# Optimization experiments

Measured on AMD Instinct MI355X. Metric: run time of the kernel, lower is better.

The kernel has to match this reference:

```python
import jax, jax.numpy as jnp
import numpy as np

D_MODEL = 1024
NUM_HEADS = 16
B, S = 1, 4096


def setup_inputs() -> dict:
    key = jax.random.key(0)
    kx, kq, kk, kv, ko = jax.random.split(key, 5)
    std = (1.0 / D_MODEL) ** 0.5
    def trunc(k):
        return std * jax.random.truncated_normal(k, -3.0, 3.0, (D_MODEL, D_MODEL), dtype=jnp.float32)
    return {
        "x": jax.random.normal(kx, (B, S, D_MODEL), dtype=jnp.float32),
        "W_Q": trunc(kq),
        "W_K": trunc(kk),
        "W_V": trunc(kv),
        "W_O": trunc(ko),
    }


def reference(x, W_Q, W_K, W_V, W_O):
    Bx, Sx, Dm = x.shape
    H = NUM_HEADS
    d_attn = Dm // H
    # projections (torch code uses x @ W.T)
    Q = x @ W_Q.T
    K = x @ W_K.T
    V = x @ W_V.T
    # [B, H, S, d]
    Q = Q.reshape(Bx, Sx, H, d_attn).transpose(0, 2, 1, 3)
    K = K.reshape(Bx, Sx, H, d_attn).transpose(0, 2, 1, 3)
    V = V.reshape(Bx, Sx, H, d_attn).transpose(0, 2, 1, 3)
    scale = 1.0 / jnp.sqrt(jnp.asarray(d_attn, dtype=x.dtype))
    # [B, H, S, S] scores
    attn = jnp.einsum("bhqd,bhkd->bhqk", Q, K) * scale
    causal = jnp.tril(jnp.ones((Sx, Sx), dtype=bool))
    attn = jnp.where(causal, attn, jnp.asarray(-jnp.inf, dtype=attn.dtype))
    probs = jax.nn.softmax(attn, axis=-1)
    y = jnp.einsum("bhqk,bhkd->bhqd", probs, V)
    y = y.transpose(0, 2, 1, 3).reshape(Bx, Sx, Dm)
    return y @ W_O.T
```

## Files before the change

### kernel.cpp

```cpp
#include <hip/hip_runtime.h>

#define S_LEN 4096
#define DMODEL 1024
#define NHEADS 16

typedef __attribute__((ext_vector_type(8))) short bf16x8;
typedef __attribute__((ext_vector_type(4))) float f32x4;
typedef unsigned short u16;
typedef unsigned int u32;
typedef unsigned long long u64;

__device__ inline u16 f2bf(float f) {
    union { float f; u32 u; } v; v.f = f;
    u32 r = v.u + 0x7fffu + ((v.u >> 16) & 1u);
    return (u16)(r >> 16);
}

__device__ inline u32 pkbf2(float a, float b) {
    union { float f; u32 u; } ua, ub; ua.f = a; ub.f = b;
    const u32 ra = ua.u + 0x7fffu + ((ua.u >> 16) & 1u);
    const u32 rb = ub.u + 0x7fffu + ((ub.u >> 16) & 1u);
    return __builtin_amdgcn_perm(rb, ra, 0x07060302u);
}

__device__ inline u32 pkbf2f(float a, float b) {
    union { float f; u32 u; } ua, ub; ua.f = a; ub.f = b;
    const u32 ra = ua.u + 0x8000u;
    const u32 rb = ub.u + 0x8000u;
    return __builtin_amdgcn_perm(rb, ra, 0x07060302u);
}

__device__ inline void cp16(const void* g, void* l) {
    __builtin_amdgcn_global_load_lds(
        (const __attribute__((address_space(1))) unsigned int*)g,
        (__attribute__((address_space(3))) unsigned int*)l, 16, 0, 0);
}

__global__ __launch_bounds__(256) void cvt_all(const float* __restrict__ x,
                                               const float* __restrict__ wq,
                                               const float* __restrict__ wk,
                                               const float* __restrict__ wv,
                                               const float* __restrict__ wo,
                                               u16* __restrict__ xb,
                                               u16* __restrict__ w3,
                                               u16* __restrict__ wob) {
    const int b = blockIdx.x;
    const float* s; u16* d; int off;
    const int NW = DMODEL * DMODEL;
    if (b < 2048)      { s = x;  d = xb;          off = b * 2048; }
    else if (b < 2560) { s = wq; d = w3;          off = (b - 2048) * 2048; }
    else if (b < 3072) { s = wk; d = w3 + NW;     off = (b - 2560) * 2048; }
    else if (b < 3584) { s = wv; d = w3 + 2 * NW; off = (b - 3072) * 2048; }
    else               { s = wo; d = wob;         off = (b - 3584) * 2048; }
    const int i = off + threadIdx.x * 8;
    const float4 a = *(const float4*)(s + i);
    const float4 c = *(const float4*)(s + i + 4);
    u16 t[8];
    t[0] = f2bf(a.x); t[1] = f2bf(a.y); t[2] = f2bf(a.z); t[3] = f2bf(a.w);
    t[4] = f2bf(c.x); t[5] = f2bf(c.y); t[6] = f2bf(c.z); t[7] = f2bf(c.w);
    *(bf16x8*)(d + i) = *(const bf16x8*)t;
}

__global__ __launch_bounds__(256) void gemm_qkv(const u16* __restrict__ A,
                                                const u16* __restrict__ B3,
                                                u16* __restrict__ Qo,
                                                u16* __restrict__ Ko,
                                                u16* __restrict__ Vo) {
    __shared__ __align__(16) u16 As[2][128 * 32];
    __shared__ __align__(16) u16 Bs[2][128 * 32];
    const int tid = threadIdx.x, lane = tid & 63, wave = tid >> 6;
    const int wm = (wave >> 1) * 64, wn = (wave & 1) * 64;
    const int m0 = blockIdx.y * 128, n0 = blockIdx.x * 128;
    const int l15 = lane & 15, quad = lane >> 4;

    f32x4 acc[4][4];
#pragma unroll
    for (int i = 0; i < 4; i++)
#pragma unroll
        for (int j = 0; j < 4; j++) acc[i][j] = (f32x4){0.f, 0.f, 0.f, 0.f};

    const int r0 = tid >> 2, c0 = (tid & 3) * 8;

    cp16(A + (size_t)(m0 + r0) * 1024 + c0,       As[0] + r0 * 32 + c0);
    cp16(A + (size_t)(m0 + r0 + 64) * 1024 + c0,  As[0] + (r0 + 64) * 32 + c0);
    cp16(B3 + (size_t)(n0 + r0) * 1024 + c0,      Bs[0] + r0 * 32 + c0);
    cp16(B3 + (size_t)(n0 + r0 + 64) * 1024 + c0, Bs[0] + (r0 + 64) * 32 + c0);

    int cur = 0;
    for (int kk = 0; kk < 1024; kk += 32) {
        __syncthreads();
        if (kk + 32 < 1024) {
            const int kn = kk + 32;
            cp16(A + (size_t)(m0 + r0) * 1024 + kn + c0,       As[cur ^ 1] + r0 * 32 + c0);
            cp16(A + (size_t)(m0 + r0 + 64) * 1024 + kn + c0,  As[cur ^ 1] + (r0 + 64) * 32 + c0);
            cp16(B3 + (size_t)(n0 + r0) * 1024 + kn + c0,      Bs[cur ^ 1] + r0 * 32 + c0);
            cp16(B3 + (size_t)(n0 + r0 + 64) * 1024 + kn + c0, Bs[cur ^ 1] + (r0 + 64) * 32 + c0);
        }
        bf16x8 af[4], bfr[4];
#pragma unroll
        for (int i = 0; i < 4; i++)
            af[i] = *(const bf16x8*)(As[cur] + (wm + i * 16 + l15) * 32 + quad * 8);
#pragma unroll
        for (int j = 0; j < 4; j++)
            bfr[j] = *(const bf16x8*)(Bs[cur] + (wn + j * 16 + l15) * 32 + quad * 8);
#pragma unroll
        for (int i = 0; i < 4; i++)
#pragma unroll
            for (int j = 0; j < 4; j++)
                acc[i][j] = __builtin_amdgcn_mfma_f32_16x16x32_bf16(af[i], bfr[j], acc[i][j], 0, 0, 0);
        cur ^= 1;
    }

    const int which = n0 >> 10;
    const int n0r = n0 & 1023;
    u16* dst = (which == 0) ? Qo : (which == 1) ? Ko : Vo;
    const float sc = (which == 0) ? 0.125f * 1.4426950408889634f : 1.0f;
#pragma unroll
    for (int i = 0; i < 4; i++)
#pragma unroll
        for (int j = 0; j < 4; j++)
#pragma unroll
            for (int r = 0; r < 4; r++) {
                const int row = m0 + wm + i * 16 + quad * 4 + r;
                const int col = n0r + wn + j * 16 + l15;
                const int h = col >> 6, c = col & 63;
                const u16 v = f2bf(acc[i][j][r] * sc);
                if (which < 2) dst[(size_t)h * S_LEN * 64 + (size_t)row * 64 + c] = v;
                else           dst[(size_t)h * S_LEN * 64 + (size_t)c * S_LEN + row] = v;
            }
}

__global__ __launch_bounds__(256) void gemm_out(const u16* __restrict__ A,
                                                const u16* __restrict__ B,
                                                float* __restrict__ C) {
    __shared__ __align__(16) u16 As[2][64 * 64];
    __shared__ __align__(16) u16 Bs[2][128 * 64];
    const int tid = threadIdx.x, lane = tid & 63, wave = tid >> 6;
    const int wm = (wave >> 1) * 32, wn = (wave & 1) * 64;
    const int bx = blockIdx.x;
    const int n0 = (bx & 7) * 128, m0 = (bx >> 3) * 64;
    const int l15 = lane & 15, quad = lane >> 4;
    const int swz = l15 & 7;

    f32x4 acc[2][4];
#pragma unroll
    for (int i = 0; i < 2; i++)
#pragma unroll
        for (int j = 0; j < 4; j++) acc[i][j] = (f32x4){0.f, 0.f, 0.f, 0.f};

#define STAGE_OUT(buf, kb)                                                              \
    {                                                                                   \
        _Pragma("unroll")                                                               \
        for (int q = 0; q < 2; q++) {                                                   \
            const int ch = tid + q * 256;                                               \
            const int ar = ch >> 3, ac = ((ch & 7) ^ (ar & 7)) * 8;                     \
            cp16(A + (size_t)(m0 + ar) * 1024 + (kb) + ac, As[buf] + ch * 8);           \
        }                                                                               \
        _Pragma("unroll")                                                               \
        for (int q = 0; q < 4; q++) {                                                   \
            const int ch = tid + q * 256;                                               \
            const int br = ch >> 3, bc = ((ch & 7) ^ (br & 7)) * 8;                     \
            cp16(B + (size_t)(n0 + br) * 1024 + (kb) + bc, Bs[buf] + ch * 8);           \
        }                                                                               \
    }

    STAGE_OUT(0, 0);
    int cur = 0;
    for (int kk = 0; kk < 1024; kk += 64) {
        __syncthreads();
        if (kk + 64 < 1024) STAGE_OUT(cur ^ 1, kk + 64);
#pragma unroll
        for (int h = 0; h < 2; h++) {
            const int cc = (h * 4 + quad) ^ swz;
            bf16x8 af[2], bfr[4];
#pragma unroll
            for (int i = 0; i < 2; i++)
                af[i] = *(const bf16x8*)(As[cur] + (wm + i * 16 + l15) * 64 + cc * 8);
#pragma unroll
            for (int j = 0; j < 4; j++)
                bfr[j] = *(const bf16x8*)(Bs[cur] + (wn + j * 16 + l15) * 64 + cc * 8);
#pragma unroll
            for (int i = 0; i < 2; i++)
#pragma unroll
                for (int j = 0; j < 4; j++)
                    acc[i][j] = __builtin_amdgcn_mfma_f32_16x16x32_bf16(af[i], bfr[j], acc[i][j], 0, 0, 0);
        }
        cur ^= 1;
    }
#undef STAGE_OUT

#pragma unroll
    for (int i = 0; i < 2; i++)
#pragma unroll
        for (int j = 0; j < 4; j++)
#pragma unroll
            for (int r = 0; r < 4; r++) {
                const int row = m0 + wm + i * 16 + quad * 4 + r;
                const int col = n0 + wn + j * 16 + l15;
                C[(size_t)row * 1024 + col] = acc[i][j][r];
            }
}

__global__ __launch_bounds__(256, 2) void attn(const u16* __restrict__ Q,
                                               const u16* __restrict__ Kh,
                                               const u16* __restrict__ Vt,
                                               u16* __restrict__ Y) {
    __shared__ __align__(16) u16 Ks[2][128 * 64];
    __shared__ __align__(16) u16 Vs[2][64 * 128];
    const int b = blockIdx.x;
    const int head = b & 15;
    const int jq = 63 - (b >> 4);
    const int nkt = jq + 1;
    const int np = (nkt + 1) >> 1;
    const int qa = jq * 64;
    const int tid = threadIdx.x, lane = tid & 63, w = tid >> 6;
    const int l15 = lane & 15, quad = lane >> 4;
    const int swz = l15 & 7;

    const u16* Qp = Q + (size_t)head * S_LEN * 64;
    const u16* Kp = Kh + (size_t)head * S_LEN * 64;
    const u16* Vp = Vt + (size_t)head * 64 * S_LEN;

    bf16x8 qf[4][2];
#pragma unroll
    for (int qg = 0; qg < 4; qg++)
#pragma unroll
        for (int h = 0; h < 2; h++)
            qf[qg][h] = *(const bf16x8*)(Qp + (size_t)(qa + qg * 16 + l15) * 64 + h * 32 + quad * 8);

    f32x4 o[4][4];
#pragma unroll
    for (int dg = 0; dg < 4; dg++)
#pragma unroll
        for (int qg = 0; qg < 4; qg++) o[dg][qg] = (f32x4){0.f, 0.f, 0.f, 0.f};
    float lp[4] = {0.f, 0.f, 0.f, 0.f};

#define STAGE_PAIR(buf, kp2)                                                       \
    {                                                                              \
        _Pragma("unroll")                                                          \
        for (int q = 0; q < 4; q++) {                                              \
            const int ch = tid + q * 256;                                          \
            const int kr = ch >> 3, kc = ((ch & 7) ^ (kr & 7)) * 8;                \
            cp16(Kp + (size_t)((kp2) * 128 + kr) * 64 + kc, Ks[buf] + ch * 8);     \
            const int vr = ch >> 4, lc = ch & 15;                                  \
            const int vc = ((lc & 8) | ((lc & 7) ^ (vr & 7))) * 8;                 \
            cp16(Vp + (size_t)vr * S_LEN + (kp2) * 128 + vc, Vs[buf] + ch * 8);    \
        }                                                                          \
    }

    STAGE_PAIR(0, 0);
    int cur = 0;
    for (int kp = 0; kp < np; kp++) {
        __syncthreads();
        if (kp + 1 < np) STAGE_PAIR(cur ^ 1, kp + 1);
        const u16* K_ = Ks[cur];
        const u16* V_ = Vs[cur];
        const bool hasO = (2 * kp + 1 < nkt);
        const bool diagE = (2 * kp == jq);
        const bool diagO = (2 * kp + 1 == jq);

        const int rE = w * 16 + l15;
        const bf16x8 kE0 = *(const bf16x8*)(K_ + rE * 64 + (quad ^ swz) * 8);
        const bf16x8 kE1 = *(const bf16x8*)(K_ + rE * 64 + ((4 + quad) ^ swz) * 8);
        bf16x8 kO0, kO1;
        if (hasO) {
            kO0 = *(const bf16x8*)(K_ + (rE + 64) * 64 + (quad ^ swz) * 8);
            kO1 = *(const bf16x8*)(K_ + (rE + 64) * 64 + ((4 + quad) ^ swz) * 8);
        }

        const int keyl = w * 16 + quad * 4;
        union { u32 d[4]; bf16x8 v; } pu[4];
#pragma unroll
        for (int qg = 0; qg < 4; qg++) {
            const int ql = qg * 16 + l15;
            f32x4 cE = (f32x4){0.f, 0.f, 0.f, 0.f};
            cE = __builtin_amdgcn_mfma_f32_16x16x32_bf16(kE0, qf[qg][0], cE, 0, 0, 0);
            cE = __builtin_amdgcn_mfma_f32_16x16x32_bf16(kE1, qf[qg][1], cE, 0, 0, 0);
            float p0 = __builtin_amdgcn_exp2f(cE[0]);
            float p1 = __builtin_amdgcn_exp2f(cE[1]);
            float p2 = __builtin_amdgcn_exp2f(cE[2]);
            float p3 = __builtin_amdgcn_exp2f(cE[3]);
            if (diagE) {
                if (keyl + 0 > ql) p0 = 0.f;
                if (keyl + 1 > ql) p1 = 0.f;
                if (keyl + 2 > ql) p2 = 0.f;
                if (keyl + 3 > ql) p3 = 0.f;
            }
            lp[qg] += (p0 + p1) + (p2 + p3);
            pu[qg].d[0] = pkbf2f(p0, p1);
            pu[qg].d[1] = pkbf2f(p2, p3);
            if (hasO) {
                f32x4 cO = (f32x4){0.f, 0.f, 0.f, 0.f};
                cO = __builtin_amdgcn_mfma_f32_16x16x32_bf16(kO0, qf[qg][0], cO, 0, 0, 0);
                cO = __builtin_amdgcn_mfma_f32_16x16x32_bf16(kO1, qf[qg][1], cO, 0, 0, 0);
                float q0 = __builtin_amdgcn_exp2f(cO[0]);
                float q1 = __builtin_amdgcn_exp2f(cO[1]);
                float q2 = __builtin_amdgcn_exp2f(cO[2]);
                float q3 = __builtin_amdgcn_exp2f(cO[3]);
                if (diagO) {
                    if (keyl + 0 > ql) q0 = 0.f;
                    if (keyl + 1 > ql) q1 = 0.f;
                    if (keyl + 2 > ql) q2 = 0.f;
                    if (keyl + 3 > ql) q3 = 0.f;
                }
                lp[qg] += (q0 + q1) + (q2 + q3);
                pu[qg].d[2] = pkbf2f(q0, q1);
                pu[qg].d[3] = pkbf2f(q2, q3);
            } else {
                pu[qg].d[2] = 0u;
                pu[qg].d[3] = 0u;
            }
        }

#pragma unroll
        for (int dg = 0; dg < 4; dg++) {
            const int vrow = dg * 16 + l15;
            const int gcE = w * 2 + (quad >> 1);
            const int sc = gcE ^ swz;
            union { u64 d[2]; bf16x8 v; } vf;
            vf.d[0] = *(const u64*)(V_ + vrow * 128 + sc * 8 + (quad & 1) * 4);
            vf.d[1] = hasO ? *(const u64*)(V_ + vrow * 128 + (8 | sc) * 8 + (quad & 1) * 4)
                           : 0ull;
#pragma unroll
            for (int qg = 0; qg < 4; qg++)
                o[dg][qg] = __builtin_amdgcn_mfma_f32_16x16x32_bf16(vf.v, pu[qg].v, o[dg][qg], 0, 0, 0);
        }
        cur ^= 1;
    }
#undef STAGE_PAIR

#pragma unroll
    for (int qg = 0; qg < 4; qg++) {
        lp[qg] += __shfl_xor(lp[qg], 16);
        lp[qg] += __shfl_xor(lp[qg], 32);
    }
    __syncthreads();
    float* OR = (float*)&Ks[0][0];
    float* LR = (float*)&Vs[0][0];
    if (lane < 16) {
#pragma unroll
        for (int qg = 0; qg < 4; qg++) LR[(w * 4 + qg) * 16 + lane] = lp[qg];
    }
#pragma unroll
    for (int c = 0; c < 2; c++) {
        if (c) __syncthreads();
#pragma unroll
        for (int d2 = 0; d2 < 2; d2++)
#pragma unroll
            for (int qg = 0; qg < 4; qg++)
                *(f32x4*)&OR[(((w * 2 + d2) * 4 + qg) * 16 + l15) * 16 + quad * 4] = o[c * 2 + d2][qg];
        __syncthreads();
        const int d2r = w >> 1, qh = w & 1;
        const int qrow = qh * 32 + (lane >> 1);
        const int qg = qrow >> 4, lq = qrow & 15;
        const int dd = (lane & 1) * 8;
        f32x4 sa = (f32x4){0.f, 0.f, 0.f, 0.f};
        f32x4 sb = (f32x4){0.f, 0.f, 0.f, 0.f};
#pragma unroll
        for (int sw = 0; sw < 4; sw++) {
            const float* p = &OR[(((sw * 2 + d2r) * 4 + qg) * 16 + lq) * 16 + dd];
            sa += *(const f32x4*)p;
            sb += *(const f32x4*)(p + 4);
        }
        const float l = LR[qg * 16 + lq] + LR[(4 + qg) * 16 + lq] +
                        LR[(8 + qg) * 16 + lq] + LR[(12 + qg) * 16 + lq];
        const float inv = 1.f / l;
        const int dg = c * 2 + d2r;
        union { u32 d[4]; bf16x8 v; } yv;
        yv.d[0] = pkbf2(sa[0] * inv, sa[1] * inv);
        yv.d[1] = pkbf2(sa[2] * inv, sa[3] * inv);
        yv.d[2] = pkbf2(sb[0] * inv, sb[1] * inv);
        yv.d[3] = pkbf2(sb[2] * inv, sb[3] * inv);
        *(bf16x8*)(Y + (size_t)(qa + qrow) * DMODEL + head * 64 + dg * 16 + dd) = yv.v;
    }
}

extern "C" void kernel_launch(void* const* d_in, const int* in_sizes, int n_in,
                              void* d_out, int out_size, void* d_ws, size_t ws_size,
                              hipStream_t stream) {
    const float* x  = (const float*)d_in[0];
    const float* wq = (const float*)d_in[1];
    const float* wk = (const float*)d_in[2];
    const float* wv = (const float*)d_in[3];
    const float* wo = (const float*)d_in[4];
    float* out = (float*)d_out;

    u16* qh  = (u16*)d_ws;
    u16* kh  = qh + (size_t)S_LEN * DMODEL;
    u16* vt  = kh + (size_t)S_LEN * DMODEL;
    u16* xb  = vt + (size_t)S_LEN * DMODEL;
    u16* y   = xb;
    u16* wb3 = xb + (size_t)S_LEN * DMODEL;
    u16* wob = wb3 + (size_t)3 * DMODEL * DMODEL;

    const dim3 blk(256);

    cvt_all<<<4096, blk, 0, stream>>>(x, wq, wk, wv, wo, xb, wb3, wob);
    gemm_qkv<<<dim3(3 * DMODEL / 128, S_LEN / 128), blk, 0, stream>>>(xb, wb3, qh, kh, vt);
    attn<<<1024, blk, 0, stream>>>(qh, kh, vt, y);
    gemm_out<<<512, blk, 0, stream>>>(y, wob, out);
}
```

Baseline: 206.5 us.

## Load K and V fragments directly from global memory, drop LDS double-buffering

```diff
diff --git a/kernel.cpp b/kernel.cpp
--- a/kernel.cpp
+++ b/kernel.cpp
@@ -201,12 +201,12 @@
             }
 }
 
-__global__ __launch_bounds__(256, 2) void attn(const u16* __restrict__ Q,
+__global__ __launch_bounds__(256, 3) void attn(const u16* __restrict__ Q,
                                                const u16* __restrict__ Kh,
                                                const u16* __restrict__ Vt,
                                                u16* __restrict__ Y) {
-    __shared__ __align__(16) u16 Ks[2][128 * 64];
-    __shared__ __align__(16) u16 Vs[2][64 * 128];
+    __shared__ __align__(16) float OR[256 * 20];
+    __shared__ float LR[256];
     const int b = blockIdx.x;
     const int head = b & 15;
     const int jq = 63 - (b >> 4);
@@ -215,7 +215,6 @@
     const int qa = jq * 64;
     const int tid = threadIdx.x, lane = tid & 63, w = tid >> 6;
     const int l15 = lane & 15, quad = lane >> 4;
-    const int swz = l15 & 7;
 
     const u16* Qp = Q + (size_t)head * S_LEN * 64;
     const u16* Kp = Kh + (size_t)head * S_LEN * 64;
@@ -235,51 +234,37 @@
         for (int qg = 0; qg < 4; qg++) o[dg][qg] = (f32x4){0.f, 0.f, 0.f, 0.f};
     float lp[4] = {0.f, 0.f, 0.f, 0.f};
 
-#define STAGE_PAIR(buf, kp2)                                                       \
-    {                                                                              \
-        _Pragma("unroll")                                                          \
-        for (int q = 0; q < 4; q++) {                                              \
-            const int ch = tid + q * 256;                                          \
-            const int kr = ch >> 3, kc = ((ch & 7) ^ (kr & 7)) * 8;                \
-            cp16(Kp + (size_t)((kp2) * 128 + kr) * 64 + kc, Ks[buf] + ch * 8);     \
-            const int vr = ch >> 4, lc = ch & 15;                                  \
-            const int vc = ((lc & 8) | ((lc & 7) ^ (vr & 7))) * 8;                 \
-            cp16(Vp + (size_t)vr * S_LEN + (kp2) * 128 + vc, Vs[buf] + ch * 8);    \
-        }                                                                          \
-    }
-
-    STAGE_PAIR(0, 0);
-    int cur = 0;
+    const u16* kpe = Kp + (size_t)(w * 16 + l15) * 64 + quad * 8;
+    const u16* vp0 = Vp + (size_t)l15 * S_LEN + w * 16 + quad * 4;
+    const u16* vp1 = vp0 + (size_t)16 * S_LEN;
+    const u16* vp2 = vp0 + (size_t)32 * S_LEN;
+    const u16* vp3 = vp0 + (size_t)48 * S_LEN;
+
+    const int keyl = w * 16 + quad * 4;
+
     for (int kp = 0; kp < np; kp++) {
-        __syncthreads();
-        if (kp + 1 < np) STAGE_PAIR(cur ^ 1, kp + 1);
-        const u16* K_ = Ks[cur];
-        const u16* V_ = Vs[cur];
+        const bf16x8 kE0 = *(const bf16x8*)(kpe);
+        const bf16x8 kE1 = *(const bf16x8*)(kpe + 32);
+        const bf16x8 kO0 = *(const bf16x8*)(kpe + 64 * 64);
+        const bf16x8 kO1 = *(const bf16x8*)(kpe + 64 * 64 + 32);
+        kpe += 128 * 64;
         const bool hasO = (2 * kp + 1 < nkt);
         const bool diagE = (2 * kp == jq);
         const bool diagO = (2 * kp + 1 == jq);
 
-        const int rE = w * 16 + l15;
-        const bf16x8 kE0 = *(const bf16x8*)(K_ + rE * 64 + (quad ^ swz) * 8);
-        const bf16x8 kE1 = *(const bf16x8*)(K_ + rE * 64 + ((4 + quad) ^ swz) * 8);
-        bf16x8 kO0, kO1;
-        if (hasO) {
-            kO0 = *(const bf16x8*)(K_ + (rE + 64) * 64 + (quad ^ swz) * 8);
-            kO1 = *(const bf16x8*)(K_ + (rE + 64) * 64 + ((4 + quad) ^ swz) * 8);
-        }
-
-        const int keyl = w * 16 + quad * 4;
-        union { u32 d[4]; bf16x8 v; } pu[4];
+        union VU { u64 d[2]; bf16x8 v; };
+        union PU { u32 d[4]; bf16x8 v; } pu[4];
+
 #pragma unroll
         for (int qg = 0; qg < 4; qg++) {
             const int ql = qg * 16 + l15;
-            f32x4 cE = (f32x4){0.f, 0.f, 0.f, 0.f};
-            cE = __builtin_amdgcn_mfma_f32_16x16x32_bf16(kE0, qf[qg][0], cE, 0, 0, 0);
-            cE = __builtin_amdgcn_mfma_f32_16x16x32_bf16(kE1, qf[qg][1], cE, 0, 0, 0);
-            float p0 = __builtin_amdgcn_exp2f(cE[0]);
-            float p1 = __builtin_amdgcn_exp2f(cE[1]);
-            float p2 = __builtin_amdgcn_exp2f(cE[2]);
-            float p3 = __builtin_amdgcn_exp2f(cE[3]);
+            f32x4 c = (f32x4){0.f, 0.f, 0.f, 0.f};
+            c = __builtin_amdgcn_mfma_f32_16x16x32_bf16(kE0, qf[qg][0], c, 0, 0, 0);
+            c = __builtin_amdgcn_mfma_f32_16x16x32_bf16(kE1, qf[qg][1], c, 0, 0, 0);
+            float p0 = __builtin_amdgcn_exp2f(c[0]);
+            float p1 = __builtin_amdgcn_exp2f(c[1]);
+            float p2 = __builtin_amdgcn_exp2f(c[2]);
+            float p3 = __builtin_amdgcn_exp2f(c[3]);
             if (diagE) {
                 if (keyl + 0 > ql) p0 = 0.f;
                 if (keyl + 1 > ql) p1 = 0.f;
@@ -289,89 +274,86 @@
             lp[qg] += (p0 + p1) + (p2 + p3);
             pu[qg].d[0] = pkbf2f(p0, p1);
             pu[qg].d[1] = pkbf2f(p2, p3);
-            if (hasO) {
-                f32x4 cO = (f32x4){0.f, 0.f, 0.f, 0.f};
-                cO = __builtin_amdgcn_mfma_f32_16x16x32_bf16(kO0, qf[qg][0], cO, 0, 0, 0);
-                cO = __builtin_amdgcn_mfma_f32_16x16x32_bf16(kO1, qf[qg][1], cO, 0, 0, 0);
-                float q0 = __builtin_amdgcn_exp2f(cO[0]);
-                float q1 = __builtin_amdgcn_exp2f(cO[1]);
-                float q2 = __builtin_amdgcn_exp2f(cO[2]);
-                float q3 = __builtin_amdgcn_exp2f(cO[3]);
+        }
+
+        VU v0, v1, v2, v3;
+        v0.d[0] = *(const u64*)(vp0); v0.d[1] = *(const u64*)(vp0 + 64); vp0 += 128;
+        v1.d[0] = *(const u64*)(vp1); v1.d[1] = *(const u64*)(vp1 + 64); vp1 += 128;
+
+        if (hasO) {
+#pragma unroll
+            for (int qg = 0; qg < 4; qg++) {
+                const int ql = qg * 16 + l15;
+                f32x4 c = (f32x4){0.f, 0.f, 0.f, 0.f};
+                c = __builtin_amdgcn_mfma_f32_16x16x32_bf16(kO0, qf[qg][0], c, 0, 0, 0);
+                c = __builtin_amdgcn_mfma_f32_16x16x32_bf16(kO1, qf[qg][1], c, 0, 0, 0);
+                float p0 = __builtin_amdgcn_exp2f(c[0]);
+                float p1 = __builtin_amdgcn_exp2f(c[1]);
+                float p2 = __builtin_amdgcn_exp2f(c[2]);
+                float p3 = __builtin_amdgcn_exp2f(c[3]);
                 if (diagO) {
-                    if (keyl + 0 > ql) q0 = 0.f;
-                    if (keyl + 1 > ql) q1 = 0.f;
-                    if (keyl + 2 > ql) q2 = 0.f;
-                    if (keyl + 3 > ql) q3 = 0.f;
+                    if (keyl + 0 > ql) p0 = 0.f;
+                    if (keyl + 1 > ql) p1 = 0.f;
+                    if (keyl + 2 > ql) p2 = 0.f;
+                    if (keyl + 3 > ql) p3 = 0.f;
                 }
-                lp[qg] += (q0 + q1) + (q2 + q3);
-                pu[qg].d[2] = pkbf2f(q0, q1);
-                pu[qg].d[3] = pkbf2f(q2, q3);
-            } else {
-                pu[qg].d[2] = 0u;
-                pu[qg].d[3] = 0u;
+                lp[qg] += (p0 + p1) + (p2 + p3);
+                pu[qg].d[2] = pkbf2f(p0, p1);
+                pu[qg].d[3] = pkbf2f(p2, p3);
             }
+        } else {
+#pragma unroll
+            for (int qg = 0; qg < 4; qg++) { pu[qg].d[2] = 0u; pu[qg].d[3] = 0u; }
         }
 
-#pragma unroll
-        for (int dg = 0; dg < 4; dg++) {
-            const int vrow = dg * 16 + l15;
-            const int gcE = w * 2 + (quad >> 1);
-            const int sc = gcE ^ swz;
-            union { u64 d[2]; bf16x8 v; } vf;
-            vf.d[0] = *(const u64*)(V_ + vrow * 128 + sc * 8 + (quad & 1) * 4);
-            vf.d[1] = hasO ? *(const u64*)(V_ + vrow * 128 + (8 | sc) * 8 + (quad & 1) * 4)
-                           : 0ull;
-#pragma unroll
-            for (int qg = 0; qg < 4; qg++)
-                o[dg][qg] = __builtin_amdgcn_mfma_f32_16x16x32_bf16(vf.v, pu[qg].v, o[dg][qg], 0, 0, 0);
-        }
-        cur ^= 1;
-    }
-#undef STAGE_PAIR
+        v2.d[0] = *(const u64*)(vp2); v2.d[1] = *(const u64*)(vp2 + 64); vp2 += 128;
+        v3.d[0] = *(const u64*)(vp3); v3.d[1] = *(const u64*)(vp3 + 64); vp3 += 128;
+
+#pragma unroll
+        for (int qg = 0; qg < 4; qg++)
+            o[0][qg] = __builtin_amdgcn_mfma_f32_16x16x32_bf16(v0.v, pu[qg].v, o[0][qg], 0, 0, 0);
+#pragma unroll
+        for (int qg = 0; qg < 4; qg++)
+            o[1][qg] = __builtin_amdgcn_mfma_f32_16x16x32_bf16(v1.v, pu[qg].v, o[1][qg], 0, 0, 0);
+#pragma unroll
+        for (int qg = 0; qg < 4; qg++)
+            o[2][qg] = __builtin_amdgcn_mfma_f32_16x16x32_bf16(v2.v, pu[qg].v, o[2][qg], 0, 0, 0);
+#pragma unroll
+        for (int qg = 0; qg < 4; qg++)
+            o[3][qg] = __builtin_amdgcn_mfma_f32_16x16x32_bf16(v3.v, pu[qg].v, o[3][qg], 0, 0, 0);
+    }
 
 #pragma unroll
     for (int qg = 0; qg < 4; qg++) {
         lp[qg] += __shfl_xor(lp[qg], 16);
         lp[qg] += __shfl_xor(lp[qg], 32);
     }
+    if (lane < 16) {
+#pragma unroll
+        for (int qg = 0; qg < 4; qg++) LR[(w * 4 + qg) * 16 + lane] = lp[qg];
+    }
+    const int qrow = tid >> 2;
+    const int qgr = qrow >> 4, lq = qrow & 15;
+    const int dpart = (tid & 3) * 4;
     __syncthreads();
-    float* OR = (float*)&Ks[0][0];
-    float* LR = (float*)&Vs[0][0];
-    if (lane < 16) {
-#pragma unroll
-        for (int qg = 0; qg < 4; qg++) LR[(w * 4 + qg) * 16 + lane] = lp[qg];
-    }
-#pragma unroll
-    for (int c = 0; c < 2; c++) {
-        if (c) __syncthreads();
-#pragma unroll
-        for (int d2 = 0; d2 < 2; d2++)
-#pragma unroll
-            for (int qg = 0; qg < 4; qg++)
-                *(f32x4*)&OR[(((w * 2 + d2) * 4 + qg) * 16 + l15) * 16 + quad * 4] = o[c * 2 + d2][qg];
+    const float lsum = LR[qgr * 16 + lq] + LR[(4 + qgr) * 16 + lq] +
+                       LR[(8 + qgr) * 16 + lq] + LR[(12 + qgr) * 16 + lq];
+    const float inv = 1.f / lsum;
+#pragma unroll
+    for (int dg = 0; dg < 4; dg++) {
+        if (dg) __syncthreads();
+#pragma unroll
+        for (int qg = 0; qg < 4; qg++)
+            *(f32x4*)&OR[((w * 4 + qg) * 16 + l15) * 20 + quad * 4] = o[dg][qg];
         __syncthreads();
-        const int d2r = w >> 1, qh = w & 1;
-        const int qrow = qh * 32 + (lane >> 1);
-        const int qg = qrow >> 4, lq = qrow & 15;
-        const int dd = (lane & 1) * 8;
-        f32x4 sa = (f32x4){0.f, 0.f, 0.f, 0.f};
-        f32x4 sb = (f32x4){0.f, 0.f, 0.f, 0.f};
-#pragma unroll
-        for (int sw = 0; sw < 4; sw++) {
-            const float* p = &OR[(((sw * 2 + d2r) * 4 + qg) * 16 + lq) * 16 + dd];
-            sa += *(const f32x4*)p;
-            sb += *(const f32x4*)(p + 4);
-        }
-        const float l = LR[qg * 16 + lq] + LR[(4 + qg) * 16 + lq] +
-                        LR[(8 + qg) * 16 + lq] + LR[(12 + qg) * 16 + lq];
-        const float inv = 1.f / l;
-        const int dg = c * 2 + d2r;
-        union { u32 d[4]; bf16x8 v; } yv;
-        yv.d[0] = pkbf2(sa[0] * inv, sa[1] * inv);
-        yv.d[1] = pkbf2(sa[2] * inv, sa[3] * inv);
-        yv.d[2] = pkbf2(sb[0] * inv, sb[1] * inv);
-        yv.d[3] = pkbf2(sb[2] * inv, sb[3] * inv);
-        *(bf16x8*)(Y + (size_t)(qa + qrow) * DMODEL + head * 64 + dg * 16 + dd) = yv.v;
+        f32x4 s = (f32x4){0.f, 0.f, 0.f, 0.f};
+#pragma unroll
+        for (int sw = 0; sw < 4; sw++)
+            s += *(const f32x4*)&OR[((sw * 4 + qgr) * 16 + lq) * 20 + dpart];
+        const u32 y0 = pkbf2(s[0] * inv, s[1] * inv);
+        const u32 y1 = pkbf2(s[2] * inv, s[3] * inv);
+        *(u64*)(Y + (size_t)(qa + qrow) * DMODEL + head * 64 + dg * 16 + dpart) =
+            (u64)y0 | ((u64)y1 << 32);
     }
 }
 
```

New measurement: 246.2 us. 1.19x slower.
